# Kernel optimization log

Measured on AMD Instinct MI355X. Metric: run time of the kernel, lower is better.

The kernel has to match this reference:

```python
import jax, jax.numpy as jnp
import numpy as np

N_T = 3
TAU = 1.0 / (N_T - 1)


def setup_inputs() -> dict:
    key = jax.random.key(0)
    k1, k2, k3 = jax.random.split(key, 3)
    B, n_src, n_tgt = 4, 2048, 2048
    momentum = jax.random.normal(k1, (B, n_src, 2), dtype=jnp.float32)
    source_init = jax.random.normal(k2, (B, n_src, 2), dtype=jnp.float32)
    target_init = jax.random.normal(k3, (B, n_tgt, 2), dtype=jnp.float32)
    sigmaV2 = jnp.ones((), dtype=jnp.float32)
    return {"momentum": momentum, "source_init": source_init,
            "target_init": target_init, "sigmaV2": sigmaV2}


def _rbf_aggregate(x, mom, sigmaV2):
    # x: [B, n_pt, 2] landmark locations; mom: [B, n_pt, 2] momenta
    # w[b,i,j] = exp(-||x_i - x_j||^2 / sigmaV2); dp[b,i,:] = sum_j w[b,i,j] * mom[b,j,:]
    d2 = jnp.sum((x[:, :, None, :] - x[:, None, :, :]) ** 2, axis=-1)  # [B,n,n]
    w = jnp.exp(-d2 / sigmaV2)
    return jnp.einsum('bij,bjd->bid', w, mom)


def reference(momentum, source_init, target_init, sigmaV2):
    B = momentum.shape[0]
    n_momentum = momentum.reshape(B, -1, 2).shape[1]
    land = jnp.concatenate([source_init, target_init], axis=1)  # [B, n_pt, 2]
    mom = jnp.zeros_like(land).at[:, :n_momentum].set(momentum.reshape(B, -1, 2))
    # two Euler steps of the RBF-kernel flow
    dp1 = _rbf_aggregate(land, mom, sigmaV2)
    shape1 = land + dp1 * TAU
    dp2 = _rbf_aggregate(shape1, mom, sigmaV2)
    out = shape1 + dp2 * TAU
    return out[:, n_momentum:]
```

## Files before the change

kernel.cpp:

```cpp
#include <hip/hip_runtime.h>


constexpr int N     = 2048;
constexpr int TPB   = 256;
constexpr int MP    = 4;
constexpr int PPB   = (TPB / 64) * MP;
constexpr int NJ    = N / 64;
constexpr float TAU   = 0.5f;
constexpr float LOG2E = 1.44269504088896340736f;

__device__ inline float exp2_neg(float x) {
    return __builtin_amdgcn_exp2f(-x);
}

template<int STEP>
__global__ __launch_bounds__(TPB, 4)
void deform_kernel(const float* __restrict__ momentum,
                   const float* __restrict__ source_init,
                   const float* __restrict__ target_init,
                   const float* __restrict__ sigmaV2,
                   float* __restrict__ shape1,
                   float* __restrict__ out)
{
    __shared__ float4 sj[N];

    const int tid  = threadIdx.x;
    const int ppb  = (STEP == 1) ? 2 * N : N;
    const int bpb  = ppb / PPB;
    const int b    = blockIdx.x / bpb;
    const int pblk = blockIdx.x % bpb;

    const float scale = sqrtf(LOG2E / sigmaV2[0]);

    for (int k4 = tid; k4 < N / 2; k4 += TPB) {
        float4 p;
        if (STEP == 1) p = ((const float4*)source_init)[b * (N / 2) + k4];
        else           p = ((const float4*)(shape1 + (size_t)b * 2 * N * 2))[k4];
        const float4 m = ((const float4*)momentum)[b * (N / 2) + k4];
        sj[2 * k4 + 0] = make_float4(p.x * scale, p.y * scale, m.x * TAU, m.y * TAU);
        sj[2 * k4 + 1] = make_float4(p.z * scale, p.w * scale, m.z * TAU, m.w * TAU);
    }

    const int lane = tid & 63;
    const int g    = tid >> 6;
    const int pi0  = pblk * PPB + g * MP;

    float4 pa, pb;
    if (STEP == 1) {
        if (pi0 < N) {
            pa = ((const float4*)source_init)[(b * N + pi0) >> 1];
            pb = ((const float4*)source_init)[(b * N + pi0 + 2) >> 1];
        } else {
            pa = ((const float4*)target_init)[(b * N + (pi0 - N)) >> 1];
            pb = ((const float4*)target_init)[(b * N + (pi0 - N) + 2) >> 1];
        }
    } else {
        pa = ((const float4*)shape1)[(b * 2 * N + N + pi0) >> 1];
        pb = ((const float4*)shape1)[(b * 2 * N + N + pi0 + 2) >> 1];
    }
    const float xs[MP] = {pa.x * scale, pa.z * scale, pb.x * scale, pb.z * scale};
    const float ys[MP] = {pa.y * scale, pa.w * scale, pb.y * scale, pb.w * scale};
    __syncthreads();

    float ax[MP] = {0.f, 0.f, 0.f, 0.f};
    float ay[MP] = {0.f, 0.f, 0.f, 0.f};
    #pragma unroll 4
    for (int t = 0; t < NJ; ++t) {
        const float4 s = sj[t * 64 + lane];
        #pragma unroll
        for (int m = 0; m < MP; ++m) {
            const float dx = xs[m] - s.x;
            const float dy = ys[m] - s.y;
            const float w  = exp2_neg(fmaf(dy, dy, dx * dx));
            ax[m] = fmaf(w, s.z, ax[m]);
            ay[m] = fmaf(w, s.w, ay[m]);
        }
    }

    #pragma unroll
    for (int d = 1; d < 64; d <<= 1) {
        #pragma unroll
        for (int m = 0; m < MP; ++m) {
            ax[m] += __shfl_xor(ax[m], d);
            ay[m] += __shfl_xor(ay[m], d);
        }
    }

    if (lane == 0) {
        const float4 o0 = make_float4(pa.x + ax[0], pa.y + ay[0],
                                      pa.z + ax[1], pa.w + ay[1]);
        const float4 o1 = make_float4(pb.x + ax[2], pb.y + ay[2],
                                      pb.z + ax[3], pb.w + ay[3]);
        if (STEP == 1) {
            ((float4*)shape1)[(b * 2 * N + pi0) >> 1]     = o0;
            ((float4*)shape1)[(b * 2 * N + pi0 + 2) >> 1] = o1;
        } else {
            ((float4*)out)[(b * N + pi0) >> 1]     = o0;
            ((float4*)out)[(b * N + pi0 + 2) >> 1] = o1;
        }
    }
}

extern "C" void kernel_launch(void* const* d_in, const int* in_sizes, int n_in,
                              void* d_out, int out_size, void* d_ws, size_t ws_size,
                              hipStream_t stream)
{
    const float* momentum    = (const float*)d_in[0];
    const float* source_init = (const float*)d_in[1];
    const float* target_init = (const float*)d_in[2];
    const float* sigmaV2     = (const float*)d_in[3];
    float* out    = (float*)d_out;
    float* shape1 = (float*)d_ws;

    const int B = in_sizes[0] / (N * 2);

    dim3 blk(TPB);
    deform_kernel<1><<<dim3(B * (2 * N / PPB)), blk, 0, stream>>>(
        momentum, source_init, target_init, sigmaV2, shape1, out);
    deform_kernel<2><<<dim3(B * (N / PPB)), blk, 0, stream>>>(
        momentum, source_init, target_init, sigmaV2, shape1, out);
}
```

Baseline: 21.56 us.

## Fuse both Euler steps into one kernel with per-batch atomic counter handoff

```diff
diff --git a/kernel.cpp b/kernel.cpp
--- a/kernel.cpp
+++ b/kernel.cpp
@@ -1,11 +1,15 @@
 #include <hip/hip_runtime.h>
 
 
-constexpr int N     = 2048;
-constexpr int TPB   = 256;
-constexpr int MP    = 4;
-constexpr int PPB   = (TPB / 64) * MP;
-constexpr int NJ    = N / 64;
+typedef unsigned int u32;
+
+constexpr int N    = 2048;
+constexpr int TPB  = 256;
+constexpr int MP   = 4;
+constexpr int PPA  = (TPB / 64) * MP;
+constexpr int NJ   = N / 64;
+constexpr int BPB  = 2 * N / PPA;
+constexpr int SRCB = N / PPA;
 constexpr float TAU   = 0.5f;
 constexpr float LOG2E = 1.44269504088896340736f;
 
@@ -13,91 +17,135 @@
     return __builtin_amdgcn_exp2f(-x);
 }
 
-template<int STEP>
 __global__ __launch_bounds__(TPB, 4)
-void deform_kernel(const float* __restrict__ momentum,
-                   const float* __restrict__ source_init,
-                   const float* __restrict__ target_init,
-                   const float* __restrict__ sigmaV2,
-                   float* __restrict__ shape1,
-                   float* __restrict__ out)
+void deform_fused(const float* __restrict__ momentum,
+                  const float* __restrict__ source_init,
+                  const float* __restrict__ target_init,
+                  const float* __restrict__ sigmaV2,
+                  float* __restrict__ ws_sxy,
+                  u32*   __restrict__ cnt,
+                  float* __restrict__ out)
 {
-    __shared__ float4 sj[N];
+    __shared__ float2 sxy[N];
+    __shared__ float2 smo[N];
 
     const int tid  = threadIdx.x;
-    const int ppb  = (STEP == 1) ? 2 * N : N;
-    const int bpb  = ppb / PPB;
-    const int b    = blockIdx.x / bpb;
-    const int pblk = blockIdx.x % bpb;
+    const int b    = blockIdx.x / BPB;
+    const int r    = blockIdx.x % BPB;
+    const bool is_src = (r < SRCB);
+    const int pblk = is_src ? r : r - SRCB;
 
     const float scale = sqrtf(LOG2E / sigmaV2[0]);
 
     for (int k4 = tid; k4 < N / 2; k4 += TPB) {
-        float4 p;
-        if (STEP == 1) p = ((const float4*)source_init)[b * (N / 2) + k4];
-        else           p = ((const float4*)(shape1 + (size_t)b * 2 * N * 2))[k4];
-        const float4 m = ((const float4*)momentum)[b * (N / 2) + k4];
-        sj[2 * k4 + 0] = make_float4(p.x * scale, p.y * scale, m.x * TAU, m.y * TAU);
-        sj[2 * k4 + 1] = make_float4(p.z * scale, p.w * scale, m.z * TAU, m.w * TAU);
+        const float4 p = ((const float4*)source_init)[b * (N / 2) + k4];
+        const float4 m = ((const float4*)momentum  )[b * (N / 2) + k4];
+        sxy[2 * k4 + 0] = make_float2(p.x * scale, p.y * scale);
+        sxy[2 * k4 + 1] = make_float2(p.z * scale, p.w * scale);
+        smo[2 * k4 + 0] = make_float2(m.x * TAU, m.y * TAU);
+        smo[2 * k4 + 1] = make_float2(m.z * TAU, m.w * TAU);
     }
 
     const int lane = tid & 63;
     const int g    = tid >> 6;
-    const int pi0  = pblk * PPB + g * MP;
+    const int pi0  = pblk * PPA + g * MP;
 
-    float4 pa, pb;
-    if (STEP == 1) {
-        if (pi0 < N) {
-            pa = ((const float4*)source_init)[(b * N + pi0) >> 1];
-            pb = ((const float4*)source_init)[(b * N + pi0 + 2) >> 1];
-        } else {
-            pa = ((const float4*)target_init)[(b * N + (pi0 - N)) >> 1];
-            pb = ((const float4*)target_init)[(b * N + (pi0 - N) + 2) >> 1];
-        }
-    } else {
-        pa = ((const float4*)shape1)[(b * 2 * N + N + pi0) >> 1];
-        pb = ((const float4*)shape1)[(b * 2 * N + N + pi0 + 2) >> 1];
-    }
-    const float xs[MP] = {pa.x * scale, pa.z * scale, pb.x * scale, pb.z * scale};
-    const float ys[MP] = {pa.y * scale, pa.w * scale, pb.y * scale, pb.w * scale};
+    const float* ibase = is_src ? source_init : target_init;
+    const float4 pa  = ((const float4*)ibase)[(b * N + pi0) >> 1];
+    const float4 pb4 = ((const float4*)ibase)[(b * N + pi0 + 2) >> 1];
+    float xr[MP] = {pa.x, pa.z, pb4.x, pb4.z};
+    float yr[MP] = {pa.y, pa.w, pb4.y, pb4.w};
+    float xs[MP], ys[MP];
+    #pragma unroll
+    for (int m = 0; m < MP; ++m) { xs[m] = xr[m] * scale; ys[m] = yr[m] * scale; }
     __syncthreads();
 
-    float ax[MP] = {0.f, 0.f, 0.f, 0.f};
-    float ay[MP] = {0.f, 0.f, 0.f, 0.f};
+    float ax[MP] = {0, 0, 0, 0}, ay[MP] = {0, 0, 0, 0};
     #pragma unroll 4
     for (int t = 0; t < NJ; ++t) {
-        const float4 s = sj[t * 64 + lane];
+        const float2 s  = sxy[t * 64 + lane];
+        const float2 mo = smo[t * 64 + lane];
         #pragma unroll
         for (int m = 0; m < MP; ++m) {
-            const float dx = xs[m] - s.x;
-            const float dy = ys[m] - s.y;
+            const float dx = xs[m] - s.x, dy = ys[m] - s.y;
             const float w  = exp2_neg(fmaf(dy, dy, dx * dx));
-            ax[m] = fmaf(w, s.z, ax[m]);
-            ay[m] = fmaf(w, s.w, ay[m]);
+            ax[m] = fmaf(w, mo.x, ax[m]);  ay[m] = fmaf(w, mo.y, ay[m]);
         }
     }
-
     #pragma unroll
     for (int d = 1; d < 64; d <<= 1) {
         #pragma unroll
         for (int m = 0; m < MP; ++m) {
-            ax[m] += __shfl_xor(ax[m], d);
-            ay[m] += __shfl_xor(ay[m], d);
+            ax[m] += __shfl_xor(ax[m], d);  ay[m] += __shfl_xor(ay[m], d);
         }
     }
+    #pragma unroll
+    for (int m = 0; m < MP; ++m) { xr[m] += ax[m]; yr[m] += ay[m]; }
 
+    u32* c = cnt + b * 16;
+
+    if (is_src) {
+        if (lane == 0) {
+            const float4 o0 = make_float4(xr[0] * scale, yr[0] * scale,
+                                          xr[1] * scale, yr[1] * scale);
+            const float4 o1 = make_float4(xr[2] * scale, yr[2] * scale,
+                                          xr[3] * scale, yr[3] * scale);
+            ((float4*)ws_sxy)[(b * N + pi0) >> 1]     = o0;
+            ((float4*)ws_sxy)[(b * N + pi0 + 2) >> 1] = o1;
+        }
+        __syncthreads();
+        if (tid == 0) {
+            __builtin_amdgcn_fence(__ATOMIC_RELEASE, "agent");
+            __hip_atomic_fetch_add(c, 1u, __ATOMIC_RELAXED, __HIP_MEMORY_SCOPE_AGENT);
+        }
+        return;
+    }
+
+    if (tid == 0) {
+        while (__hip_atomic_load(c, __ATOMIC_RELAXED, __HIP_MEMORY_SCOPE_AGENT)
+               < (u32)SRCB) {
+            __builtin_amdgcn_s_sleep(2);
+        }
+    }
+    __syncthreads();
+    __builtin_amdgcn_fence(__ATOMIC_ACQUIRE, "agent");
+
+    for (int k4 = tid; k4 < N / 2; k4 += TPB) {
+        const float4 p = ((const float4*)ws_sxy)[b * (N / 2) + k4];
+        sxy[2 * k4 + 0] = make_float2(p.x, p.y);
+        sxy[2 * k4 + 1] = make_float2(p.z, p.w);
+    }
+    float xsB[MP], ysB[MP];
+    #pragma unroll
+    for (int m = 0; m < MP; ++m) { xsB[m] = xr[m] * scale; ysB[m] = yr[m] * scale; }
+    __syncthreads();
+
+    float bx[MP] = {0, 0, 0, 0}, by[MP] = {0, 0, 0, 0};
+    #pragma unroll 4
+    for (int t = 0; t < NJ; ++t) {
+        const float2 s  = sxy[t * 64 + lane];
+        const float2 mo = smo[t * 64 + lane];
+        #pragma unroll
+        for (int m = 0; m < MP; ++m) {
+            const float dx = xsB[m] - s.x, dy = ysB[m] - s.y;
+            const float w  = exp2_neg(fmaf(dy, dy, dx * dx));
+            bx[m] = fmaf(w, mo.x, bx[m]);  by[m] = fmaf(w, mo.y, by[m]);
+        }
+    }
+    #pragma unroll
+    for (int d = 1; d < 64; d <<= 1) {
+        #pragma unroll
+        for (int m = 0; m < MP; ++m) {
+            bx[m] += __shfl_xor(bx[m], d);  by[m] += __shfl_xor(by[m], d);
+        }
+    }
     if (lane == 0) {
-        const float4 o0 = make_float4(pa.x + ax[0], pa.y + ay[0],
-                                      pa.z + ax[1], pa.w + ay[1]);
-        const float4 o1 = make_float4(pb.x + ax[2], pb.y + ay[2],
-                                      pb.z + ax[3], pb.w + ay[3]);
-        if (STEP == 1) {
-            ((float4*)shape1)[(b * 2 * N + pi0) >> 1]     = o0;
-            ((float4*)shape1)[(b * 2 * N + pi0 + 2) >> 1] = o1;
-        } else {
-            ((float4*)out)[(b * N + pi0) >> 1]     = o0;
-            ((float4*)out)[(b * N + pi0 + 2) >> 1] = o1;
-        }
+        const float4 o0 = make_float4(xr[0] + bx[0], yr[0] + by[0],
+                                      xr[1] + bx[1], yr[1] + by[1]);
+        const float4 o1 = make_float4(xr[2] + bx[2], yr[2] + by[2],
+                                      xr[3] + bx[3], yr[3] + by[3]);
+        ((float4*)out)[(b * N + pi0) >> 1]     = o0;
+        ((float4*)out)[(b * N + pi0 + 2) >> 1] = o1;
     }
 }
 
@@ -109,14 +157,15 @@
     const float* source_init = (const float*)d_in[1];
     const float* target_init = (const float*)d_in[2];
     const float* sigmaV2     = (const float*)d_in[3];
-    float* out    = (float*)d_out;
-    float* shape1 = (float*)d_ws;
+    float* out = (float*)d_out;
 
     const int B = in_sizes[0] / (N * 2);
 
-    dim3 blk(TPB);
-    deform_kernel<1><<<dim3(B * (2 * N / PPB)), blk, 0, stream>>>(
-        momentum, source_init, target_init, sigmaV2, shape1, out);
-    deform_kernel<2><<<dim3(B * (N / PPB)), blk, 0, stream>>>(
-        momentum, source_init, target_init, sigmaV2, shape1, out);
+    float* ws_sxy = (float*)d_ws;
+    u32*   cnt    = (u32*)((char*)d_ws + (size_t)B * N * 2 * sizeof(float));
+
+    (void)hipMemsetAsync(cnt, 0, (size_t)B * 16 * sizeof(u32), stream);
+
+    deform_fused<<<dim3(B * BPB), dim3(TPB), 0, stream>>>(
+        momentum, source_init, target_init, sigmaV2, ws_sxy, cnt, out);
 }
```

After: 62.52 us. +190.0%, slower.

## Pack source tiles as x/y pairs for packed-FP32 math; shrink step-2 MP

Applied to the files above, without the earlier changes.

```diff
diff --git a/kernel.cpp b/kernel.cpp
--- a/kernel.cpp
+++ b/kernel.cpp
@@ -1,11 +1,11 @@
 #include <hip/hip_runtime.h>
 
 
-constexpr int N     = 2048;
-constexpr int TPB   = 256;
-constexpr int MP    = 4;
-constexpr int PPB   = (TPB / 64) * MP;
-constexpr int NJ    = N / 64;
+typedef float v2f __attribute__((ext_vector_type(2)));
+
+constexpr int N    = 2048;
+constexpr int TPB  = 256;
+constexpr int NJP  = N / 2 / 64;
 constexpr float TAU   = 0.5f;
 constexpr float LOG2E = 1.44269504088896340736f;
 
@@ -13,7 +13,7 @@
     return __builtin_amdgcn_exp2f(-x);
 }
 
-template<int STEP>
+template<int STEP, int MP>
 __global__ __launch_bounds__(TPB, 4)
 void deform_kernel(const float* __restrict__ momentum,
                    const float* __restrict__ source_init,
@@ -22,11 +22,14 @@
                    float* __restrict__ shape1,
                    float* __restrict__ out)
 {
-    __shared__ float4 sj[N];
+    __shared__ float4 sjx[N / 2];
+    __shared__ float4 sjm[N / 2];
+
+    constexpr int PPA = (TPB / 64) * MP;
 
     const int tid  = threadIdx.x;
     const int ppb  = (STEP == 1) ? 2 * N : N;
-    const int bpb  = ppb / PPB;
+    const int bpb  = ppb / PPA;
     const int b    = blockIdx.x / bpb;
     const int pblk = blockIdx.x % bpb;
 
@@ -37,46 +40,68 @@
         if (STEP == 1) p = ((const float4*)source_init)[b * (N / 2) + k4];
         else           p = ((const float4*)(shape1 + (size_t)b * 2 * N * 2))[k4];
         const float4 m = ((const float4*)momentum)[b * (N / 2) + k4];
-        sj[2 * k4 + 0] = make_float4(p.x * scale, p.y * scale, m.x * TAU, m.y * TAU);
-        sj[2 * k4 + 1] = make_float4(p.z * scale, p.w * scale, m.z * TAU, m.w * TAU);
+        sjx[k4] = make_float4(p.x * scale, p.z * scale, p.y * scale, p.w * scale);
+        sjm[k4] = make_float4(m.x * TAU, m.z * TAU, m.y * TAU, m.w * TAU);
     }
 
     const int lane = tid & 63;
     const int g    = tid >> 6;
-    const int pi0  = pblk * PPB + g * MP;
+    const int pi0  = pblk * PPA + g * MP;
 
-    float4 pa, pb;
-    if (STEP == 1) {
-        if (pi0 < N) {
-            pa = ((const float4*)source_init)[(b * N + pi0) >> 1];
-            pb = ((const float4*)source_init)[(b * N + pi0 + 2) >> 1];
+    float xi[MP], yi[MP];
+    #pragma unroll
+    for (int m = 0; m < MP; ++m) {
+        float2 p;
+        if (STEP == 1) {
+            if (pi0 < N) p = ((const float2*)source_init)[b * N + pi0 + m];
+            else         p = ((const float2*)target_init)[b * N + (pi0 - N) + m];
         } else {
-            pa = ((const float4*)target_init)[(b * N + (pi0 - N)) >> 1];
-            pb = ((const float4*)target_init)[(b * N + (pi0 - N) + 2) >> 1];
+            p = ((const float2*)shape1)[b * 2 * N + N + pi0 + m];
         }
-    } else {
-        pa = ((const float4*)shape1)[(b * 2 * N + N + pi0) >> 1];
-        pb = ((const float4*)shape1)[(b * 2 * N + N + pi0 + 2) >> 1];
+        xi[m] = p.x;  yi[m] = p.y;
     }
-    const float xs[MP] = {pa.x * scale, pa.z * scale, pb.x * scale, pb.z * scale};
-    const float ys[MP] = {pa.y * scale, pa.w * scale, pb.y * scale, pb.w * scale};
+    v2f xs2[MP], ys2[MP];
+    #pragma unroll
+    for (int m = 0; m < MP; ++m) {
+        const float xs = xi[m] * scale, ys = yi[m] * scale;
+        xs2[m].x = xs;  xs2[m].y = xs;
+        ys2[m].x = ys;  ys2[m].y = ys;
+    }
     __syncthreads();
 
-    float ax[MP] = {0.f, 0.f, 0.f, 0.f};
-    float ay[MP] = {0.f, 0.f, 0.f, 0.f};
+    v2f ax2[MP], ay2[MP];
+    #pragma unroll
+    for (int m = 0; m < MP; ++m) {
+        ax2[m].x = 0.f; ax2[m].y = 0.f;
+        ay2[m].x = 0.f; ay2[m].y = 0.f;
+    }
     #pragma unroll 4
-    for (int t = 0; t < NJ; ++t) {
-        const float4 s = sj[t * 64 + lane];
+    for (int t = 0; t < NJP; ++t) {
+        const float4 sx = sjx[t * 64 + lane];
+        const float4 sm = sjm[t * 64 + lane];
+        v2f X, Y, MX, MY;
+        X.x = sx.x;  X.y = sx.y;   Y.x = sx.z;  Y.y = sx.w;
+        MX.x = sm.x; MX.y = sm.y;  MY.x = sm.z; MY.y = sm.w;
         #pragma unroll
         for (int m = 0; m < MP; ++m) {
-            const float dx = xs[m] - s.x;
-            const float dy = ys[m] - s.y;
-            const float w  = exp2_neg(fmaf(dy, dy, dx * dx));
-            ax[m] = fmaf(w, s.z, ax[m]);
-            ay[m] = fmaf(w, s.w, ay[m]);
+            const v2f dx = xs2[m] - X;
+            const v2f dy = ys2[m] - Y;
+            v2f d2 = dx * dx;
+            d2 += dy * dy;
+            v2f w;
+            w.x = exp2_neg(d2.x);
+            w.y = exp2_neg(d2.y);
+            ax2[m] += w * MX;
+            ay2[m] += w * MY;
         }
     }
 
+    float ax[MP], ay[MP];
+    #pragma unroll
+    for (int m = 0; m < MP; ++m) {
+        ax[m] = ax2[m].x + ax2[m].y;
+        ay[m] = ay2[m].x + ay2[m].y;
+    }
     #pragma unroll
     for (int d = 1; d < 64; d <<= 1) {
         #pragma unroll
@@ -87,16 +112,11 @@
     }
 
     if (lane == 0) {
-        const float4 o0 = make_float4(pa.x + ax[0], pa.y + ay[0],
-                                      pa.z + ax[1], pa.w + ay[1]);
-        const float4 o1 = make_float4(pb.x + ax[2], pb.y + ay[2],
-                                      pb.z + ax[3], pb.w + ay[3]);
-        if (STEP == 1) {
-            ((float4*)shape1)[(b * 2 * N + pi0) >> 1]     = o0;
-            ((float4*)shape1)[(b * 2 * N + pi0 + 2) >> 1] = o1;
-        } else {
-            ((float4*)out)[(b * N + pi0) >> 1]     = o0;
-            ((float4*)out)[(b * N + pi0 + 2) >> 1] = o1;
+        #pragma unroll
+        for (int m = 0; m < MP; ++m) {
+            const float2 o = make_float2(xi[m] + ax[m], yi[m] + ay[m]);
+            if (STEP == 1) ((float2*)shape1)[b * 2 * N + pi0 + m] = o;
+            else           ((float2*)out)[b * N + pi0 + m] = o;
         }
     }
 }
@@ -115,8 +135,8 @@
     const int B = in_sizes[0] / (N * 2);
 
     dim3 blk(TPB);
-    deform_kernel<1><<<dim3(B * (2 * N / PPB)), blk, 0, stream>>>(
+    deform_kernel<1, 4><<<dim3(B * (2 * N / 16)), blk, 0, stream>>>(
         momentum, source_init, target_init, sigmaV2, shape1, out);
-    deform_kernel<2><<<dim3(B * (N / PPB)), blk, 0, stream>>>(
+    deform_kernel<2, 2><<<dim3(B * (N / 8)), blk, 0, stream>>>(
         momentum, source_init, target_init, sigmaV2, shape1, out);
 }
```

After: 20.15 us. 6.5% less time.
